# Kernel tuning notes

Measured on AMD Instinct MI355X. Metric: run time of the kernel, lower is better.

## Reference

```python
import jax, jax.numpy as jnp
import numpy as np

N_EMBED = 1024
N_HEAD = 16
SEQ = 2048
BATCH = 2


def setup_inputs() -> dict:
    key = jax.random.key(0)
    ks = jax.random.split(key, 5)
    scale_in = 1.0 / np.sqrt(N_EMBED)
    x = jax.random.normal(ks[0], (BATCH, SEQ, N_EMBED), dtype=jnp.float32)
    # attn_proj: Linear(n_embed, 3*n_embed); stored as [in, out] so y = x @ W + b
    W_qkv = jax.random.normal(ks[1], (N_EMBED, 3 * N_EMBED), dtype=jnp.float32) * scale_in
    b_qkv = jax.random.normal(ks[2], (3 * N_EMBED,), dtype=jnp.float32) * 0.01
    # fin_proj: Linear(n_embed, n_embed)
    W_out = jax.random.normal(ks[3], (N_EMBED, N_EMBED), dtype=jnp.float32) * scale_in
    b_out = jax.random.normal(ks[4], (N_EMBED,), dtype=jnp.float32) * 0.01
    return {"x": x, "W_qkv": W_qkv, "b_qkv": b_qkv, "W_out": W_out, "b_out": b_out}


def reference(x, W_qkv, b_qkv, W_out, b_out):
    B, S, D = x.shape
    H = N_HEAD
    hd = D // H
    qkv = x @ W_qkv + b_qkv  # [B, S, 3D]
    q, k, v = jnp.split(qkv, 3, axis=-1)
    # [B, H, S, hd]
    q = q.reshape(B, S, H, hd).transpose(0, 2, 1, 3)
    k = k.reshape(B, S, H, hd).transpose(0, 2, 1, 3)
    v = v.reshape(B, S, H, hd).transpose(0, 2, 1, 3)
    scores = jnp.einsum("bhqd,bhkd->bhqk", q, k) * (1.0 / np.sqrt(hd))
    causal = jnp.tril(jnp.ones((S, S), dtype=bool))  # lower-triangular mask
    scores = jnp.where(causal[None, None], scores, -jnp.inf)
    probs = jax.nn.softmax(scores, axis=-1)
    # dropout is identity in eval mode (inference reference)
    attn = jnp.einsum("bhqk,bhkd->bhqd", probs, v)  # [B, H, S, hd]
    attn = attn.transpose(0, 2, 1, 3).reshape(B, S, D)
    return attn @ W_out + b_out
```

## Files before the change

kernel.cpp:

```cpp
#include <hip/hip_runtime.h>

typedef short bf16x8 __attribute__((ext_vector_type(8)));
typedef short bf16x4 __attribute__((ext_vector_type(4)));
typedef float f32x4 __attribute__((ext_vector_type(4)));
typedef int i32x4 __attribute__((ext_vector_type(4)));
typedef int i32x2 __attribute__((ext_vector_type(2)));

#define MFMA16x16x32(a, b, c) __builtin_amdgcn_mfma_f32_16x16x32_bf16(a, b, c, 0, 0, 0)
#define TRR(dst, a) asm volatile("ds_read_b64_tr_b16 %0, %1" : "=v"(dst) : "v"(a))

__device__ __forceinline__ unsigned short f2bf(float f) {
  union { float f; unsigned u; } v; v.f = f;
  unsigned u = v.u + 0x7FFFu + ((v.u >> 16) & 1u);
  return (unsigned short)(u >> 16);
}

__device__ __forceinline__ unsigned cvtpk(float lo, float hi) {
  unsigned r;
  asm("v_cvt_pk_bf16_f32 %0, %1, %2" : "=v"(r) : "v"(lo), "v"(hi));
  return r;
}

__device__ __forceinline__ float max3f(float a, float b, float c) {
  float d;
  asm("v_max3_f32 %0, %1, %2, %3" : "=v"(d) : "v"(a), "v"(b), "v"(c));
  return d;
}

__device__ __forceinline__ void gload16(const void* g, void* l) {
  __builtin_amdgcn_global_load_lds((const __attribute__((address_space(1))) void*)g,
                                   (__attribute__((address_space(3))) void*)l, 16, 0, 0);
}

__device__ __forceinline__ unsigned ldsoff(const void* p) {
  return (unsigned)(unsigned long long)(const __attribute__((address_space(3))) void*)p;
}

__global__ __launch_bounds__(256) void conv_bf16(const float* __restrict__ in,
                                                 unsigned short* __restrict__ out, int n8) {
  int i = blockIdx.x * 256 + threadIdx.x;
  if (i >= n8) return;
  const float4* p = reinterpret_cast<const float4*>(in + (long)i * 8);
  float4 a = p[0], b = p[1];
  i32x4 o;
  o[0] = cvtpk(a.x, a.y); o[1] = cvtpk(a.z, a.w);
  o[2] = cvtpk(b.x, b.y); o[3] = cvtpk(b.z, b.w);
  *reinterpret_cast<i32x4*>(out + (long)i * 8) = o;
}

__global__ __launch_bounds__(256) void trans_f32_bf16(const float* __restrict__ W,
                                                      unsigned short* __restrict__ Wt,
                                                      int K, int N) {
  __shared__ float tile[32][33];
  int n0 = blockIdx.x << 5, k0 = blockIdx.y << 5;
  int tx = threadIdx.x, ty = threadIdx.y;
#pragma unroll
  for (int i = 0; i < 32; i += 8)
    tile[ty + i][tx] = W[(long)(k0 + ty + i) * N + n0 + tx];
  __syncthreads();
#pragma unroll
  for (int i = 0; i < 32; i += 8)
    Wt[(long)(n0 + ty + i) * K + k0 + tx] = f2bf(tile[tx][ty + i]);
}

template <int BF16OUT>
__global__ __launch_bounds__(256) void gemm_bt(const unsigned short* __restrict__ A,
                                               const unsigned short* __restrict__ Bt,
                                               const float* __restrict__ bias,
                                               void* __restrict__ Cv,
                                               int M, int N, int K) {
  __shared__ __align__(128) unsigned short As[2][4096];
  __shared__ __align__(128) unsigned short Bs[2][4096];
  int t = threadIdx.x;
  int w = t >> 6, l = t & 63;
  int g = l >> 4, m16 = l & 15;
  int wr = w >> 1, wc = w & 1;
  int nwg = gridDim.x * gridDim.y;
  int f = blockIdx.y * gridDim.x + blockIdx.x;
  int q8 = nwg >> 3;
  int s = (f & 7) * q8 + (f >> 3);
  int bx = s % gridDim.x, by = s / gridDim.x;
  long am0 = (long)by << 7;
  long bn0 = (long)bx << 7;

  int seg0 = w, seg1 = 4 + w;
  int fl0 = (seg0 << 9) + (l << 3), fl1 = (seg1 << 9) + (l << 3);
  int r0 = fl0 >> 5, c0 = fl0 & 31;
  int r1 = fl1 >> 5, c1 = fl1 & 31;

  f32x4 acc[4][4];
#pragma unroll
  for (int i = 0; i < 4; ++i)
#pragma unroll
    for (int j = 0; j < 4; ++j) acc[i][j] = (f32x4){0.f, 0.f, 0.f, 0.f};

  gload16(A + (am0 + r0) * K + c0, &As[0][seg0 << 9]);
  gload16(A + (am0 + r1) * K + c1, &As[0][seg1 << 9]);
  gload16(Bt + (bn0 + r0) * K + c0, &Bs[0][seg0 << 9]);
  gload16(Bt + (bn0 + r1) * K + c1, &Bs[0][seg1 << 9]);

  int buf = 0;
  for (int k0 = 0; k0 < K; k0 += 32) {
    asm volatile("s_waitcnt vmcnt(0)" ::: "memory");
    __syncthreads();
    if (k0 + 32 < K) {
      int kn = k0 + 32;
      gload16(A + (am0 + r0) * K + kn + c0, &As[buf ^ 1][seg0 << 9]);
      gload16(A + (am0 + r1) * K + kn + c1, &As[buf ^ 1][seg1 << 9]);
      gload16(Bt + (bn0 + r0) * K + kn + c0, &Bs[buf ^ 1][seg0 << 9]);
      gload16(Bt + (bn0 + r1) * K + kn + c1, &Bs[buf ^ 1][seg1 << 9]);
    }
    bf16x8 af[4], bfr[4];
#pragma unroll
    for (int im = 0; im < 4; ++im)
      af[im] = *(const bf16x8*)&As[buf][((wr << 6) + (im << 4) + m16) * 32 + (g << 3)];
#pragma unroll
    for (int in = 0; in < 4; ++in)
      bfr[in] = *(const bf16x8*)&Bs[buf][((wc << 6) + (in << 4) + m16) * 32 + (g << 3)];
    __builtin_amdgcn_s_setprio(1);
#pragma unroll
    for (int im = 0; im < 4; ++im)
#pragma unroll
      for (int in = 0; in < 4; ++in)
        acc[im][in] = MFMA16x16x32(af[im], bfr[in], acc[im][in]);
    __builtin_amdgcn_s_setprio(0);
    buf ^= 1;
  }

#pragma unroll
  for (int im = 0; im < 4; ++im) {
#pragma unroll
    for (int in = 0; in < 4; ++in) {
      long col = bn0 + (wc << 6) + (in << 4) + m16;
      float bval = bias[col];
#pragma unroll
      for (int r = 0; r < 4; ++r) {
        long row = am0 + (wr << 6) + (im << 4) + (g << 2) + r;
        float v = acc[im][in][r] + bval;
        if (BF16OUT)
          ((unsigned short*)Cv)[row * N + col] = f2bf(v);
        else
          ((float*)Cv)[row * N + col] = v;
      }
    }
  }
}

__global__ __launch_bounds__(256, 3) void attn_fwd(const unsigned short* __restrict__ qkv,
                                                   unsigned short* __restrict__ out) {
  const int D3 = 3072;
  const float C1 = 0.18033688f;
  const float THR = 11.5415603f;
  __shared__ __align__(128) unsigned short Ks[2][4096];
  __shared__ __align__(128) unsigned short Vs[2][4096];
  int b = blockIdx.x >> 4, h = blockIdx.x & 15;
  int yy = blockIdx.y;
  int qt = (yy & 1) ? (31 - (yy >> 1)) : (yy >> 1);
  int t = threadIdx.x;
  int w = t >> 6, l = t & 63;
  int g = l >> 4, m16 = l & 15;
  long base = (long)b * 2048 * D3;
  const unsigned short* kbase = qkv + base + 1024 + h * 64;
  const unsigned short* vbase = qkv + base + 2048 + h * 64;

  int l8 = l >> 3, sc = l & 7;
  int kof = (w * 8 + l8) * D3 + ((sc ^ l8) << 3);
  int s0 = w * 8 + l8;
  int vof = ((s0 & 15) * 4 + (sc >> 1)) * D3 + ((s0 >> 4) << 4) + ((sc & 1) << 3);
  const f32x4 zero4 = (f32x4){0.f, 0.f, 0.f, 0.f};

  int qrow = (qt << 6) + (w << 4) + m16;
  const unsigned short* qp = qkv + base + (long)qrow * D3 + h * 64;
  bf16x8 qf0 = *(const bf16x8*)(qp + g * 8);
  bf16x8 qf1 = *(const bf16x8*)(qp + 32 + g * 8);

  f32x4 O[4];
#pragma unroll
  for (int d = 0; d < 4; ++d) O[d] = zero4;
  f32x4 lsv = zero4;
  float m2 = -1e30f;
  int nt = qt + 1;

  gload16(kbase + kof, &Ks[0][w << 9]);
  gload16(kbase + 32 * D3 + kof, &Ks[0][2048 + (w << 9)]);
  gload16(vbase + vof, &Vs[0][w << 9]);
  gload16(vbase + vof + 32, &Vs[0][2048 + (w << 9)]);

  int buf = 0;
  for (int ss = 0; ss < nt; ++ss) {
    asm volatile("s_waitcnt vmcnt(0)" ::: "memory");
    __syncthreads();
    if (ss + 1 < nt) {
      long off = (long)(ss + 1) * 64 * D3;
      gload16(kbase + off + kof, &Ks[buf ^ 1][w << 9]);
      gload16(kbase + off + 32 * D3 + kof, &Ks[buf ^ 1][2048 + (w << 9)]);
      gload16(vbase + off + vof, &Vs[buf ^ 1][w << 9]);
      gload16(vbase + off + vof + 32, &Vs[buf ^ 1][2048 + (w << 9)]);
    }

    unsigned va = ldsoff(&Vs[buf][0]) + (g << 7) + (m16 << 3);
    bf16x4 t0[4], t1[4], t2[4], t3[4];
#pragma unroll
    for (int d = 0; d < 4; ++d) {
      unsigned a = va + (d << 11);
      TRR(t0[d], a);
      TRR(t1[d], a + 512);
      TRR(t2[d], a + 1024);
      TRR(t3[d], a + 1536);
    }
    const char* kbuf = (const char*)&Ks[buf][0];
    int swz = m16 & 7;
    f32x4 st[4];
    __builtin_amdgcn_s_setprio(1);
#pragma unroll
    for (int T = 0; T < 4; ++T) {
      const char* rp = kbuf + (((T << 4) + m16) << 7);
      bf16x8 kf0 = *(const bf16x8*)(rp + ((g ^ swz) << 4));
      bf16x8 kf1 = *(const bf16x8*)(rp + (((4 + g) ^ swz) << 4));
      st[T] = MFMA16x16x32(kf0, qf0, zero4);
      st[T] = MFMA16x16x32(kf1, qf1, st[T]);
    }
    __builtin_amdgcn_s_setprio(0);

    if (ss == nt - 1) {
      int rq = qrow - (ss << 6);
#pragma unroll
      for (int T = 0; T < 4; ++T)
#pragma unroll
        for (int r = 0; r < 4; ++r)
          if ((T << 4) + (g << 2) + r > rq) st[T][r] = -3e38f;
    }
    float tm[4];
#pragma unroll
    for (int T = 0; T < 4; ++T)
      tm[T] = max3f(fmaxf(st[T][0], st[T][1]), st[T][2], st[T][3]);
    float tmax = fmaxf(max3f(tm[0], tm[1], tm[2]), tm[3]);
    tmax = fmaxf(tmax, __shfl_xor(tmax, 16));
    tmax = fmaxf(tmax, __shfl_xor(tmax, 32));
    float tsc2 = tmax * C1;
    bool skip = __all(tsc2 <= m2 + THR);
    float mnew2 = skip ? m2 : fmaxf(m2, tsc2);
    float p[4][4];
    f32x4 ts4 = zero4;
#pragma unroll
    for (int T = 0; T < 4; ++T)
#pragma unroll
      for (int r = 0; r < 4; ++r) {
        float e = __builtin_amdgcn_exp2f(fmaf(st[T][r], C1, -mnew2));
        p[T][r] = e;
        ts4[r] += e;
      }
    if (!skip) {
      float alpha = __builtin_amdgcn_exp2f(m2 - mnew2);
      lsv *= alpha;
#pragma unroll
      for (int d = 0; d < 4; ++d) O[d] *= alpha;
      m2 = mnew2;
    }
    lsv += ts4;

    i32x4 w0, w1;
    w0[0] = cvtpk(p[0][0], p[0][1]); w0[1] = cvtpk(p[0][2], p[0][3]);
    w0[2] = cvtpk(p[1][0], p[1][1]); w0[3] = cvtpk(p[1][2], p[1][3]);
    w1[0] = cvtpk(p[2][0], p[2][1]); w1[1] = cvtpk(p[2][2], p[2][3]);
    w1[2] = cvtpk(p[3][0], p[3][1]); w1[3] = cvtpk(p[3][2], p[3][3]);
    bf16x8 pb0 = __builtin_bit_cast(bf16x8, w0);
    bf16x8 pb1 = __builtin_bit_cast(bf16x8, w1);

    asm volatile("s_waitcnt lgkmcnt(0)" ::: "memory");
    __builtin_amdgcn_sched_barrier(0);

    bf16x8 vfA[4], vfB[4];
#pragma unroll
    for (int d = 0; d < 4; ++d) {
      vfA[d] = __builtin_shufflevector(t0[d], t1[d], 0, 1, 2, 3, 4, 5, 6, 7);
      vfB[d] = __builtin_shufflevector(t2[d], t3[d], 0, 1, 2, 3, 4, 5, 6, 7);
    }
    __builtin_amdgcn_s_setprio(1);
#pragma unroll
    for (int d = 0; d < 4; ++d) {
      O[d] = MFMA16x16x32(vfA[d], pb0, O[d]);
      O[d] = MFMA16x16x32(vfB[d], pb1, O[d]);
    }
    __builtin_amdgcn_s_setprio(0);
    buf ^= 1;
  }

  float s = (lsv[0] + lsv[1]) + (lsv[2] + lsv[3]);
  s += __shfl_xor(s, 16);
  s += __shfl_xor(s, 32);
  float inv = 1.0f / s;
  unsigned short* op = out + (long)(b * 2048 + qrow) * 1024 + h * 64;
#pragma unroll
  for (int d = 0; d < 4; ++d) {
    i32x2 pk;
    pk[0] = (int)cvtpk(O[d][0] * inv, O[d][1] * inv);
    pk[1] = (int)cvtpk(O[d][2] * inv, O[d][3] * inv);
    *reinterpret_cast<i32x2*>(op + (d << 4) + (g << 2)) = pk;
  }
}

extern "C" void kernel_launch(void* const* d_in, const int* in_sizes, int n_in,
                              void* d_out, int out_size, void* d_ws, size_t ws_size,
                              hipStream_t stream) {
  const float* x     = (const float*)d_in[0];
  const float* W_qkv = (const float*)d_in[1];
  const float* b_qkv = (const float*)d_in[2];
  const float* W_out = (const float*)d_in[3];
  const float* b_out = (const float*)d_in[4];

  char* ws = (char*)d_ws;
  unsigned short* xb    = (unsigned short*)ws;
  unsigned short* wqkvT = (unsigned short*)(ws + (8l << 20));
  unsigned short* woutT = (unsigned short*)(ws + (14l << 20));
  unsigned short* qkv   = (unsigned short*)(ws + (16l << 20));

  conv_bf16<<<2048, 256, 0, stream>>>(x, xb, 524288);
  trans_f32_bf16<<<dim3(96, 32), dim3(32, 8), 0, stream>>>(W_qkv, wqkvT, 1024, 3072);
  trans_f32_bf16<<<dim3(32, 32), dim3(32, 8), 0, stream>>>(W_out, woutT, 1024, 1024);
  gemm_bt<1><<<dim3(24, 32), 256, 0, stream>>>(xb, wqkvT, b_qkv, (void*)qkv, 4096, 3072, 1024);
  attn_fwd<<<dim3(32, 32), 256, 0, stream>>>(qkv, xb);
  gemm_bt<0><<<dim3(8, 32), 256, 0, stream>>>(xb, woutT, b_out, d_out, 4096, 1024, 1024);
}
```

Before: 116.0 us.

## Fuse prep kernels into one launch and triple-buffer GEMM loads

The x conversion and the two weight transpose kernels are merged into a single prep launch that dispatches on block index. This removes two kernel launches and their gaps. The GEMM moves from double to triple buffering of its LDS tiles, prefetching two k-steps ahead and waiting with vmcnt(4) so one tile's loads stay in flight while the current tile is computed. LDS use per block rises to 48KB, which may reduce occupancy.

```diff
diff --git a/kernel.cpp b/kernel.cpp
--- a/kernel.cpp
+++ b/kernel.cpp
@@ -36,24 +36,36 @@
   return (unsigned)(unsigned long long)(const __attribute__((address_space(3))) void*)p;
 }
 
-__global__ __launch_bounds__(256) void conv_bf16(const float* __restrict__ in,
-                                                 unsigned short* __restrict__ out, int n8) {
-  int i = blockIdx.x * 256 + threadIdx.x;
-  if (i >= n8) return;
-  const float4* p = reinterpret_cast<const float4*>(in + (long)i * 8);
-  float4 a = p[0], b = p[1];
-  i32x4 o;
-  o[0] = cvtpk(a.x, a.y); o[1] = cvtpk(a.z, a.w);
-  o[2] = cvtpk(b.x, b.y); o[3] = cvtpk(b.z, b.w);
-  *reinterpret_cast<i32x4*>(out + (long)i * 8) = o;
-}
-
-__global__ __launch_bounds__(256) void trans_f32_bf16(const float* __restrict__ W,
-                                                      unsigned short* __restrict__ Wt,
-                                                      int K, int N) {
+__global__ __launch_bounds__(256) void prep(const float* __restrict__ x,
+                                            unsigned short* __restrict__ xb,
+                                            const float* __restrict__ Wq,
+                                            unsigned short* __restrict__ WqT,
+                                            const float* __restrict__ Wo,
+                                            unsigned short* __restrict__ WoT) {
   __shared__ float tile[32][33];
-  int n0 = blockIdx.x << 5, k0 = blockIdx.y << 5;
-  int tx = threadIdx.x, ty = threadIdx.y;
+  int bid = blockIdx.x;
+  int t = threadIdx.x;
+  if (bid < 2048) {
+    long i = (long)bid * 256 + t;
+    const float4* p = reinterpret_cast<const float4*>(x + i * 8);
+    float4 a = p[0], b = p[1];
+    i32x4 o;
+    o[0] = cvtpk(a.x, a.y); o[1] = cvtpk(a.z, a.w);
+    o[2] = cvtpk(b.x, b.y); o[3] = cvtpk(b.z, b.w);
+    *reinterpret_cast<i32x4*>(xb + i * 8) = o;
+    return;
+  }
+  const float* W; unsigned short* Wt; int N, bx, by;
+  if (bid < 5120) {
+    W = Wq; Wt = WqT; N = 3072;
+    int r = bid - 2048; bx = r % 96; by = r / 96;
+  } else {
+    W = Wo; Wt = WoT; N = 1024;
+    int r = bid - 5120; bx = r & 31; by = r >> 5;
+  }
+  const int K = 1024;
+  int tx = t & 31, ty = t >> 5;
+  int n0 = bx << 5, k0 = by << 5;
 #pragma unroll
   for (int i = 0; i < 32; i += 8)
     tile[ty + i][tx] = W[(long)(k0 + ty + i) * N + n0 + tx];
@@ -69,8 +81,8 @@
                                                const float* __restrict__ bias,
                                                void* __restrict__ Cv,
                                                int M, int N, int K) {
-  __shared__ __align__(128) unsigned short As[2][4096];
-  __shared__ __align__(128) unsigned short Bs[2][4096];
+  __shared__ __align__(128) unsigned short As[3][4096];
+  __shared__ __align__(128) unsigned short Bs[3][4096];
   int t = threadIdx.x;
   int w = t >> 6, l = t & 63;
   int g = l >> 4, m16 = l & 15;
@@ -98,25 +110,33 @@
   gload16(A + (am0 + r1) * K + c1, &As[0][seg1 << 9]);
   gload16(Bt + (bn0 + r0) * K + c0, &Bs[0][seg0 << 9]);
   gload16(Bt + (bn0 + r1) * K + c1, &Bs[0][seg1 << 9]);
-
-  int buf = 0;
+  gload16(A + (am0 + r0) * K + 32 + c0, &As[1][seg0 << 9]);
+  gload16(A + (am0 + r1) * K + 32 + c1, &As[1][seg1 << 9]);
+  gload16(Bt + (bn0 + r0) * K + 32 + c0, &Bs[1][seg0 << 9]);
+  gload16(Bt + (bn0 + r1) * K + 32 + c1, &Bs[1][seg1 << 9]);
+
+  int cur = 0;
   for (int k0 = 0; k0 < K; k0 += 32) {
-    asm volatile("s_waitcnt vmcnt(0)" ::: "memory");
+    if (k0 + 32 < K)
+      asm volatile("s_waitcnt vmcnt(4)" ::: "memory");
+    else
+      asm volatile("s_waitcnt vmcnt(0)" ::: "memory");
     __syncthreads();
-    if (k0 + 32 < K) {
-      int kn = k0 + 32;
-      gload16(A + (am0 + r0) * K + kn + c0, &As[buf ^ 1][seg0 << 9]);
-      gload16(A + (am0 + r1) * K + kn + c1, &As[buf ^ 1][seg1 << 9]);
-      gload16(Bt + (bn0 + r0) * K + kn + c0, &Bs[buf ^ 1][seg0 << 9]);
-      gload16(Bt + (bn0 + r1) * K + kn + c1, &Bs[buf ^ 1][seg1 << 9]);
+    if (k0 + 64 < K) {
+      int kn = k0 + 64;
+      int nb = cur + 2; if (nb >= 3) nb -= 3;
+      gload16(A + (am0 + r0) * K + kn + c0, &As[nb][seg0 << 9]);
+      gload16(A + (am0 + r1) * K + kn + c1, &As[nb][seg1 << 9]);
+      gload16(Bt + (bn0 + r0) * K + kn + c0, &Bs[nb][seg0 << 9]);
+      gload16(Bt + (bn0 + r1) * K + kn + c1, &Bs[nb][seg1 << 9]);
     }
     bf16x8 af[4], bfr[4];
 #pragma unroll
     for (int im = 0; im < 4; ++im)
-      af[im] = *(const bf16x8*)&As[buf][((wr << 6) + (im << 4) + m16) * 32 + (g << 3)];
+      af[im] = *(const bf16x8*)&As[cur][((wr << 6) + (im << 4) + m16) * 32 + (g << 3)];
 #pragma unroll
     for (int in = 0; in < 4; ++in)
-      bfr[in] = *(const bf16x8*)&Bs[buf][((wc << 6) + (in << 4) + m16) * 32 + (g << 3)];
+      bfr[in] = *(const bf16x8*)&Bs[cur][((wc << 6) + (in << 4) + m16) * 32 + (g << 3)];
     __builtin_amdgcn_s_setprio(1);
 #pragma unroll
     for (int im = 0; im < 4; ++im)
@@ -124,7 +144,7 @@
       for (int in = 0; in < 4; ++in)
         acc[im][in] = MFMA16x16x32(af[im], bfr[in], acc[im][in]);
     __builtin_amdgcn_s_setprio(0);
-    buf ^= 1;
+    cur = cur == 2 ? 0 : cur + 1;
   }
 
 #pragma unroll
@@ -315,9 +335,7 @@
   unsigned short* woutT = (unsigned short*)(ws + (14l << 20));
   unsigned short* qkv   = (unsigned short*)(ws + (16l << 20));
 
-  conv_bf16<<<2048, 256, 0, stream>>>(x, xb, 524288);
-  trans_f32_bf16<<<dim3(96, 32), dim3(32, 8), 0, stream>>>(W_qkv, wqkvT, 1024, 3072);
-  trans_f32_bf16<<<dim3(32, 32), dim3(32, 8), 0, stream>>>(W_out, woutT, 1024, 1024);
+  prep<<<6144, 256, 0, stream>>>(x, xb, W_qkv, wqkvT, W_out, woutT);
   gemm_bt<1><<<dim3(24, 32), 256, 0, stream>>>(xb, wqkvT, b_qkv, (void*)qkv, 4096, 3072, 1024);
   attn_fwd<<<dim3(32, 32), 256, 0, stream>>>(qkv, xb);
   gemm_bt<0><<<dim3(8, 32), 256, 0, stream>>>(xb, woutT, b_out, d_out, 4096, 1024, 1024);
```

Result: faster. 110.4 us (-4.8%).
